# Kernel tuning notes

Measured on AMD Instinct MI355X. Metric: run time of the kernel, lower is better.

## Reference

```python
import jax, jax.numpy as jnp
import numpy as np

B, S, D_MODEL, N_HEADS, D_K, D_V = 2, 2048, 1024, 16, 64, 64


def setup_inputs() -> dict:
    key = jax.random.key(0)
    k1, k2, k3, k4, k5, k6, k7 = jax.random.split(key, 7)
    scale = 1.0 / np.sqrt(D_MODEL)
    inputs = {
        "input_Q": jax.random.normal(k1, (B, S, D_MODEL), dtype=jnp.float32),
        "input_K": jax.random.normal(k2, (B, S, D_MODEL), dtype=jnp.float32),
        "input_V": jax.random.normal(k3, (B, S, D_MODEL), dtype=jnp.float32),
        # causal mask: True means position is masked out (matches masked_fill_)
        "attn_mask": jnp.broadcast_to(
            ~jnp.tril(jnp.ones((S, S), dtype=bool)), (B, S, S)
        ),
        "flag": 0,
        "W_Q": jax.random.normal(k4, (D_MODEL, N_HEADS * D_K), dtype=jnp.float32) * scale,
        "W_K": jax.random.normal(k5, (D_MODEL, N_HEADS * D_K), dtype=jnp.float32) * scale,
        "W_V": jax.random.normal(k6, (D_MODEL, N_HEADS * D_V), dtype=jnp.float32) * scale,
        "W_O": jax.random.normal(k7, (N_HEADS * D_V, D_MODEL), dtype=jnp.float32) * scale,
    }
    return inputs


def reference(input_Q, input_K, input_V, attn_mask, flag, W_Q, W_K, W_V, W_O):
    b = input_Q.shape[0]
    # project and split heads: [b, h, s, d]
    Q = (input_Q @ W_Q).reshape(b, -1, N_HEADS, D_K).transpose(0, 2, 1, 3)
    K = (input_K @ W_K).reshape(b, -1, N_HEADS, D_K).transpose(0, 2, 1, 3)
    V = (input_V @ W_V).reshape(b, -1, N_HEADS, D_V).transpose(0, 2, 1, 3)
    # scaled dot-product attention with additive large-negative masking
    scores = jnp.einsum("bhqd,bhkd->bhqk", Q, K) / np.sqrt(D_K).astype(np.float32)
    scores = jnp.where(attn_mask[:, None, :, :], jnp.float32(-1e9), scores)
    attn = jax.nn.softmax(scores, axis=-1)
    context = jnp.einsum("bhqk,bhkd->bhqd", attn, V)  # [b, h, s, d_v]
    context = context.transpose(0, 2, 1, 3).reshape(b, -1, N_HEADS * D_V)
    return context @ W_O
```

## Files before the change

### kernel.cpp

```cpp
#include <hip/hip_runtime.h>

#define DEVINL __device__ __forceinline__

typedef __attribute__((ext_vector_type(8))) short short8;
typedef __attribute__((ext_vector_type(4))) float floatx4;

constexpr int S_LEN = 2048;
constexpr int DM    = 1024;
constexpr int NHEAD = 16;
constexpr int DHEAD = 64;
constexpr int BATCH = 2;
constexpr int MROWS = BATCH * S_LEN;
constexpr float LOG2E = 1.44269504f;
constexpr float SM_C1 = 0.125f * LOG2E;
constexpr float SM_C2 = -24.0f * LOG2E;

DEVINL unsigned short f2bf(float x) {
  union { float f; unsigned u; } un; un.f = x;
  unsigned u = un.u;
  return (unsigned short)((u + 0x7fffu + ((u >> 16) & 1u)) >> 16);
}
DEVINL unsigned short f2bf_fast(float x) {
  union { float f; unsigned u; } un; un.f = x;
  return (unsigned short)((un.u + 0x8000u) >> 16);
}

__global__ __launch_bounds__(256) void conv3_kernel(const float* __restrict__ s0,
                                                    const float* __restrict__ s1,
                                                    const float* __restrict__ s2,
                                                    unsigned short* __restrict__ d0,
                                                    unsigned short* __restrict__ d1,
                                                    unsigned short* __restrict__ d2) {
  const float* s = blockIdx.y == 0 ? s0 : (blockIdx.y == 1 ? s1 : s2);
  unsigned short* d = blockIdx.y == 0 ? d0 : (blockIdx.y == 1 ? d1 : d2);
  int i = (blockIdx.x * 256 + threadIdx.x) * 4;
  float4 v = *(const float4*)(s + i);
  unsigned lo = (unsigned)f2bf(v.x) | ((unsigned)f2bf(v.y) << 16);
  unsigned hi = (unsigned)f2bf(v.z) | ((unsigned)f2bf(v.w) << 16);
  *(uint2*)(d + i) = make_uint2(lo, hi);
}

__global__ __launch_bounds__(256) void trans4_kernel(const float* __restrict__ W0,
                                                     const float* __restrict__ W1,
                                                     const float* __restrict__ W2,
                                                     const float* __restrict__ W3,
                                                     unsigned short* __restrict__ T0,
                                                     unsigned short* __restrict__ T1,
                                                     unsigned short* __restrict__ T2,
                                                     unsigned short* __restrict__ T3) {
  const float* W = blockIdx.z == 0 ? W0 : (blockIdx.z == 1 ? W1 : (blockIdx.z == 2 ? W2 : W3));
  unsigned short* Wt = blockIdx.z == 0 ? T0 : (blockIdx.z == 1 ? T1 : (blockIdx.z == 2 ? T2 : T3));
  __shared__ unsigned short tile[32][33];
  int t = threadIdx.x;
  int c = t & 31, r0 = t >> 5;
  int nB = blockIdx.x * 32, kB = blockIdx.y * 32;
  for (int i = 0; i < 4; ++i) {
    int r = r0 + i * 8;
    tile[r][c] = f2bf(W[(size_t)(kB + r) * DM + nB + c]);
  }
  __syncthreads();
  for (int i = 0; i < 4; ++i) {
    int r = r0 + i * 8;
    Wt[(size_t)(nB + r) * DM + kB + c] = tile[c][r];
  }
}

__global__ __launch_bounds__(256) void vtrans_kernel(const unsigned short* __restrict__ vp,
                                                     unsigned short* __restrict__ vt) {
  const int bh = blockIdx.x;
  const int st = blockIdx.y;
  const int b = bh >> 4, h = bh & 15;
  const int s0 = st * 64;
  const int tid = threadIdx.x;
  __shared__ alignas(16) unsigned short tile[64 * 72];
#pragma unroll
  for (int j = 0; j < 2; ++j) {
    int ch = j * 256 + tid;
    int r = ch >> 3, c8 = (ch & 7) * 8;
    *(uint4*)&tile[r * 72 + c8] =
        *(const uint4*)&vp[((size_t)(b * S_LEN + s0 + r)) * DM + h * DHEAD + c8];
  }
  __syncthreads();
#pragma unroll
  for (int j = 0; j < 2; ++j) {
    int ch = j * 256 + tid;
    int d = ch >> 3, s8 = (ch & 7) * 8;
    unsigned short w[8];
#pragma unroll
    for (int e = 0; e < 8; ++e) w[e] = tile[(s8 + e) * 72 + d];
    *(uint4*)&vt[((size_t)(bh * DHEAD + d)) * S_LEN + s0 + s8] = *(const uint4*)w;
  }
}

DEVINL void load_lds16(const unsigned short* g, unsigned short* l) {
  __builtin_amdgcn_global_load_lds((const __attribute__((address_space(1))) unsigned int*)g,
                                   (__attribute__((address_space(3))) unsigned int*)l,
                                   16, 0, 0);
}

template <int MODE>
DEVINL void gemm_body(const unsigned short* __restrict__ A,
                      const unsigned short* __restrict__ Bt,
                      void* __restrict__ Cout) {
  constexpr int K = 1024, N = 1024;
  __shared__ alignas(16) unsigned short As[128 * 32];
  __shared__ alignas(16) unsigned short Bs[128 * 32];
  const int tid  = threadIdx.x;
  const int wave = tid >> 6, lane = tid & 63;
  const int quad = lane >> 4, l16 = lane & 15;
  const int mBase = blockIdx.y * 128, nBase = blockIdx.x * 128;
  const int wm = (wave >> 1) * 64, wn = (wave & 1) * 64;
  const int sr = lane >> 2;
  const int sc = (lane & 3) * 8;
  floatx4 acc[4][4] = {};

  for (int k0 = 0; k0 < K; k0 += 32) {
    __syncthreads();
#pragma unroll
    for (int j = 0; j < 2; ++j) {
      int row = wave * 32 + j * 16 + sr;
      load_lds16(A  + (size_t)(mBase + row) * K + k0 + sc, As + (wave * 32 + j * 16) * 32);
      load_lds16(Bt + (size_t)(nBase + row) * K + k0 + sc, Bs + (wave * 32 + j * 16) * 32);
    }
    __syncthreads();
    short8 af[4], bfr[4];
#pragma unroll
    for (int mt = 0; mt < 4; ++mt) af[mt]  = *(const short8*)&As[(wm + mt * 16 + l16) * 32 + quad * 8];
#pragma unroll
    for (int nt = 0; nt < 4; ++nt) bfr[nt] = *(const short8*)&Bs[(wn + nt * 16 + l16) * 32 + quad * 8];
#pragma unroll
    for (int mt = 0; mt < 4; ++mt)
#pragma unroll
      for (int nt = 0; nt < 4; ++nt)
        acc[mt][nt] = __builtin_amdgcn_mfma_f32_16x16x32_bf16(af[mt], bfr[nt], acc[mt][nt], 0, 0, 0);
  }

#pragma unroll
  for (int mt = 0; mt < 4; ++mt)
#pragma unroll
    for (int nt = 0; nt < 4; ++nt)
#pragma unroll
      for (int r = 0; r < 4; ++r) {
        int m = mBase + wm + mt * 16 + quad * 4 + r;
        int n = nBase + wn + nt * 16 + l16;
        if (MODE == 0) ((unsigned short*)Cout)[(size_t)m * N + n] = f2bf(acc[mt][nt][r]);
        else           ((float*)Cout)[(size_t)m * N + n]          = acc[mt][nt][r];
      }
}

__global__ __launch_bounds__(256) void gemm_qkv(const unsigned short* __restrict__ A0,
                                                const unsigned short* __restrict__ A1,
                                                const unsigned short* __restrict__ A2,
                                                const unsigned short* __restrict__ B0,
                                                const unsigned short* __restrict__ B1,
                                                const unsigned short* __restrict__ B2,
                                                unsigned short* __restrict__ C0,
                                                unsigned short* __restrict__ C1,
                                                unsigned short* __restrict__ C2) {
  const int z = blockIdx.z;
  const unsigned short* A  = z == 0 ? A0 : (z == 1 ? A1 : A2);
  const unsigned short* Bt = z == 0 ? B0 : (z == 1 ? B1 : B2);
  unsigned short* C        = z == 0 ? C0 : (z == 1 ? C1 : C2);
  gemm_body<0>(A, Bt, C);
}

__global__ __launch_bounds__(256) void gemm_out(const unsigned short* __restrict__ A,
                                                const unsigned short* __restrict__ Bt,
                                                float* __restrict__ C) {
  gemm_body<1>(A, Bt, C);
}

__global__ __launch_bounds__(256) void attn_kernel(const unsigned short* __restrict__ Qp,
                                                   const unsigned short* __restrict__ Kp,
                                                   const unsigned short* __restrict__ Vtg,
                                                   unsigned short* __restrict__ ctx) {
  const int qt = gridDim.x - 1 - blockIdx.x;
  const int bh = blockIdx.y;
  const int b  = bh >> 4, h = bh & 15;
  const int tid = threadIdx.x;
  const int wave = tid >> 6, lane = tid & 63;
  const int quad = lane >> 4, l16 = lane & 15;
  const int Q0 = qt * 128;
  const int nT = 2 * qt + 2;

  __shared__ alignas(16) unsigned short Ks[64 * 72];
  __shared__ alignas(16) unsigned short Vs[64 * 72];
  __shared__ alignas(16) unsigned short Ps[4][32 * 72];

  const unsigned short* Kbh = Kp  + (size_t)(b * S_LEN) * DM + h * DHEAD;
  const unsigned short* Vbh = Vtg + (size_t)(bh * DHEAD) * S_LEN;

  const int sr = tid >> 3, sc8 = (tid & 7) * 8;
  const unsigned short* kptr = Kbh + (size_t)sr * DM + sc8;
  const unsigned short* vptr = Vbh + (size_t)sr * S_LEN + sc8;
  unsigned short* ksl = Ks + sr * 72 + sc8;
  unsigned short* vsl = Vs + sr * 72 + sc8;

  const int rowbase = Q0 + wave * 32;
  short8 qf[2][2];
#pragma unroll
  for (int mt = 0; mt < 2; ++mt) {
    const size_t qrow = ((size_t)(b * S_LEN + rowbase + mt * 16 + l16)) * DM + h * DHEAD;
    qf[mt][0] = *(const short8*)&Qp[qrow + quad * 8];
    qf[mt][1] = *(const short8*)&Qp[qrow + 32 + quad * 8];
  }

  floatx4 o[2][4] = {};
  float rs[2][4] = {};
  unsigned short* Pw = &Ps[wave][0];

  uint4 kr0 = *(const uint4*)kptr;
  uint4 kr1 = *(const uint4*)(kptr + (size_t)32 * DM);
  uint4 vr0 = *(const uint4*)vptr;
  uint4 vr1 = *(const uint4*)(vptr + (size_t)32 * S_LEN);

  for (int t = 0; t < nT; ++t) {
    const int kb = t * 64;
    __syncthreads();
    *(uint4*)ksl              = kr0;
    *(uint4*)(ksl + 32 * 72)  = kr1;
    *(uint4*)vsl              = vr0;
    *(uint4*)(vsl + 32 * 72)  = vr1;
    __syncthreads();

    {
      const int kbn = (t + 1 < nT) ? (t + 1) * 64 : 0;
      kr0 = *(const uint4*)(kptr + (size_t)kbn * DM);
      kr1 = *(const uint4*)(kptr + (size_t)(kbn + 32) * DM);
      vr0 = *(const uint4*)(vptr + kbn);
      vr1 = *(const uint4*)(vptr + (size_t)32 * S_LEN + kbn);
    }

    floatx4 sc[2][4];
#pragma unroll
    for (int nt = 0; nt < 4; ++nt) {
      short8 kf0 = *(const short8*)&Ks[(nt * 16 + l16) * 72 + quad * 8];
      short8 kf1 = *(const short8*)&Ks[(nt * 16 + l16) * 72 + 32 + quad * 8];
#pragma unroll
      for (int mt = 0; mt < 2; ++mt) {
        floatx4 a = {};
        a = __builtin_amdgcn_mfma_f32_16x16x32_bf16(qf[mt][0], kf0, a, 0, 0, 0);
        a = __builtin_amdgcn_mfma_f32_16x16x32_bf16(qf[mt][1], kf1, a, 0, 0, 0);
        sc[mt][nt] = a;
      }
    }

    const bool masked = (t >= nT - 2);
#pragma unroll
    for (int mt = 0; mt < 2; ++mt)
#pragma unroll
      for (int nt = 0; nt < 4; ++nt) {
        const int colg = kb + nt * 16 + l16;
#pragma unroll
        for (int r = 0; r < 4; ++r) {
          float p = __builtin_amdgcn_exp2f(fmaf(sc[mt][nt][r], SM_C1, SM_C2));
          if (masked && colg > rowbase + mt * 16 + quad * 4 + r) p = 0.f;
          rs[mt][r] += p;
          Pw[(mt * 16 + quad * 4 + r) * 72 + nt * 16 + l16] = f2bf_fast(p);
        }
      }

    short8 vf[4][2];
#pragma unroll
    for (int dt = 0; dt < 4; ++dt) {
      vf[dt][0] = *(const short8*)&Vs[(dt * 16 + l16) * 72 + quad * 8];
      vf[dt][1] = *(const short8*)&Vs[(dt * 16 + l16) * 72 + 32 + quad * 8];
    }
#pragma unroll
    for (int mt = 0; mt < 2; ++mt) {
      short8 pf0 = *(const short8*)&Pw[(mt * 16 + l16) * 72 + quad * 8];
      short8 pf1 = *(const short8*)&Pw[(mt * 16 + l16) * 72 + 32 + quad * 8];
#pragma unroll
      for (int dt = 0; dt < 4; ++dt) {
        o[mt][dt] = __builtin_amdgcn_mfma_f32_16x16x32_bf16(pf0, vf[dt][0], o[mt][dt], 0, 0, 0);
        o[mt][dt] = __builtin_amdgcn_mfma_f32_16x16x32_bf16(pf1, vf[dt][1], o[mt][dt], 0, 0, 0);
      }
    }
  }

#pragma unroll
  for (int mt = 0; mt < 2; ++mt)
#pragma unroll
    for (int r = 0; r < 4; ++r) {
      float l = rs[mt][r];
#pragma unroll
      for (int off = 1; off < 16; off <<= 1) l += __shfl_xor(l, off, 64);
      float inv = 1.0f / l;
      const size_t row = (size_t)(b * S_LEN + rowbase + mt * 16 + quad * 4 + r);
#pragma unroll
      for (int dt = 0; dt < 4; ++dt)
        ctx[row * DM + h * DHEAD + dt * 16 + l16] = f2bf(o[mt][dt][r] * inv);
    }
}

extern "C" void kernel_launch(void* const* d_in, const int* in_sizes, int n_in,
                              void* d_out, int out_size, void* d_ws, size_t ws_size,
                              hipStream_t stream) {
  const float* Xq = (const float*)d_in[0];
  const float* Xk = (const float*)d_in[1];
  const float* Xv = (const float*)d_in[2];
  const float* Wq = (const float*)d_in[5];
  const float* Wk = (const float*)d_in[6];
  const float* Wv = (const float*)d_in[7];
  const float* Wo = (const float*)d_in[8];
  float* out = (float*)d_out;

  char* ws = (char*)d_ws;
  constexpr size_t XBYTES = (size_t)MROWS * DM * 2;
  constexpr size_t WBYTES = (size_t)DM * DM * 2;
  unsigned short* xq_bf = (unsigned short*)(ws);
  unsigned short* xk_bf = (unsigned short*)(ws + XBYTES);
  unsigned short* xv_bf = (unsigned short*)(ws + 2 * XBYTES);
  unsigned short* wqt   = (unsigned short*)(ws + 3 * XBYTES);
  unsigned short* wkt   = (unsigned short*)(ws + 3 * XBYTES + WBYTES);
  unsigned short* wvt   = (unsigned short*)(ws + 3 * XBYTES + 2 * WBYTES);
  unsigned short* wot   = (unsigned short*)(ws + 3 * XBYTES + 3 * WBYTES);
  unsigned short* qp    = (unsigned short*)(ws + 3 * XBYTES + 4 * WBYTES);
  unsigned short* kp    = (unsigned short*)(ws + 4 * XBYTES + 4 * WBYTES);
  unsigned short* vp    = (unsigned short*)(ws + 5 * XBYTES + 4 * WBYTES);
  unsigned short* ctx   = xq_bf;
  unsigned short* vt    = xk_bf;

  const int nX = MROWS * DM;
  conv3_kernel<<<dim3(nX / 1024, 3), 256, 0, stream>>>(Xq, Xk, Xv, xq_bf, xk_bf, xv_bf);
  trans4_kernel<<<dim3(32, 32, 4), 256, 0, stream>>>(Wq, Wk, Wv, Wo, wqt, wkt, wvt, wot);

  gemm_qkv<<<dim3(DM / 128, MROWS / 128, 3), 256, 0, stream>>>(
      xq_bf, xk_bf, xv_bf, wqt, wkt, wvt, qp, kp, vp);

  vtrans_kernel<<<dim3(BATCH * NHEAD, S_LEN / 64), 256, 0, stream>>>(vp, vt);

  attn_kernel<<<dim3(S_LEN / 128, BATCH * NHEAD), 256, 0, stream>>>(qp, kp, vt, ctx);

  gemm_out<<<dim3(DM / 128, MROWS / 128), 256, 0, stream>>>(ctx, wot, out);
}
```

Baseline: 270.5 us.

## Fuse V transpose into QKV GEMM, restructure attention to split keys across waves

```diff
diff --git a/kernel.cpp b/kernel.cpp
--- a/kernel.cpp
+++ b/kernel.cpp
@@ -3,6 +3,7 @@
 #define DEVINL __device__ __forceinline__
 
 typedef __attribute__((ext_vector_type(8))) short short8;
+typedef __attribute__((ext_vector_type(4))) short sh4;
 typedef __attribute__((ext_vector_type(4))) float floatx4;
 
 constexpr int S_LEN = 2048;
@@ -14,6 +15,8 @@
 constexpr float LOG2E = 1.44269504f;
 constexpr float SM_C1 = 0.125f * LOG2E;
 constexpr float SM_C2 = -24.0f * LOG2E;
+
+#define MFMA16(a, b, c) __builtin_amdgcn_mfma_f32_16x16x16bf16_1k(a, b, c, 0, 0, 0)
 
 DEVINL unsigned short f2bf(float x) {
   union { float f; unsigned u; } un; un.f = x;
@@ -65,33 +68,6 @@
   }
 }
 
-__global__ __launch_bounds__(256) void vtrans_kernel(const unsigned short* __restrict__ vp,
-                                                     unsigned short* __restrict__ vt) {
-  const int bh = blockIdx.x;
-  const int st = blockIdx.y;
-  const int b = bh >> 4, h = bh & 15;
-  const int s0 = st * 64;
-  const int tid = threadIdx.x;
-  __shared__ alignas(16) unsigned short tile[64 * 72];
-#pragma unroll
-  for (int j = 0; j < 2; ++j) {
-    int ch = j * 256 + tid;
-    int r = ch >> 3, c8 = (ch & 7) * 8;
-    *(uint4*)&tile[r * 72 + c8] =
-        *(const uint4*)&vp[((size_t)(b * S_LEN + s0 + r)) * DM + h * DHEAD + c8];
-  }
-  __syncthreads();
-#pragma unroll
-  for (int j = 0; j < 2; ++j) {
-    int ch = j * 256 + tid;
-    int d = ch >> 3, s8 = (ch & 7) * 8;
-    unsigned short w[8];
-#pragma unroll
-    for (int e = 0; e < 8; ++e) w[e] = tile[(s8 + e) * 72 + d];
-    *(uint4*)&vt[((size_t)(bh * DHEAD + d)) * S_LEN + s0 + s8] = *(const uint4*)w;
-  }
-}
-
 DEVINL void load_lds16(const unsigned short* g, unsigned short* l) {
   __builtin_amdgcn_global_load_lds((const __attribute__((address_space(1))) unsigned int*)g,
                                    (__attribute__((address_space(3))) unsigned int*)l,
@@ -138,14 +114,25 @@
 #pragma unroll
   for (int mt = 0; mt < 4; ++mt)
 #pragma unroll
-    for (int nt = 0; nt < 4; ++nt)
-#pragma unroll
-      for (int r = 0; r < 4; ++r) {
-        int m = mBase + wm + mt * 16 + quad * 4 + r;
-        int n = nBase + wn + nt * 16 + l16;
-        if (MODE == 0) ((unsigned short*)Cout)[(size_t)m * N + n] = f2bf(acc[mt][nt][r]);
-        else           ((float*)Cout)[(size_t)m * N + n]          = acc[mt][nt][r];
+    for (int nt = 0; nt < 4; ++nt) {
+      const int m = mBase + wm + mt * 16 + quad * 4;
+      const int n = nBase + wn + nt * 16 + l16;
+      if (MODE == 2) {
+        const int bq = m >> 11, s = m & 2047;
+        const int hh = n >> 6,  d = n & 63;
+        unsigned short w4[4];
+#pragma unroll
+        for (int r = 0; r < 4; ++r) w4[r] = f2bf(acc[mt][nt][r]);
+        *(uint2*)&((unsigned short*)Cout)[((size_t)((bq * 16 + hh) * 64 + d)) * S_LEN + s] =
+            *(const uint2*)w4;
+      } else {
+#pragma unroll
+        for (int r = 0; r < 4; ++r) {
+          if (MODE == 0) ((unsigned short*)Cout)[(size_t)(m + r) * N + n] = f2bf(acc[mt][nt][r]);
+          else           ((float*)Cout)[(size_t)(m + r) * N + n]          = acc[mt][nt][r];
+        }
       }
+    }
 }
 
 __global__ __launch_bounds__(256) void gemm_qkv(const unsigned short* __restrict__ A0,
@@ -158,139 +145,182 @@
                                                 unsigned short* __restrict__ C1,
                                                 unsigned short* __restrict__ C2) {
   const int z = blockIdx.z;
-  const unsigned short* A  = z == 0 ? A0 : (z == 1 ? A1 : A2);
-  const unsigned short* Bt = z == 0 ? B0 : (z == 1 ? B1 : B2);
-  unsigned short* C        = z == 0 ? C0 : (z == 1 ? C1 : C2);
-  gemm_body<0>(A, Bt, C);
-}
-
-__global__ __launch_bounds__(256) void gemm_out(const unsigned short* __restrict__ A,
-                                                const unsigned short* __restrict__ Bt,
-                                                float* __restrict__ C) {
-  gemm_body<1>(A, Bt, C);
-}
-
-__global__ __launch_bounds__(256) void attn_kernel(const unsigned short* __restrict__ Qp,
-                                                   const unsigned short* __restrict__ Kp,
-                                                   const unsigned short* __restrict__ Vtg,
-                                                   unsigned short* __restrict__ ctx) {
-  const int qt = gridDim.x - 1 - blockIdx.x;
+  if (z == 2)      gemm_body<2>(A2, B2, C2);
+  else if (z == 1) gemm_body<0>(A1, B1, C1);
+  else             gemm_body<0>(A0, B0, C0);
+}
+
+__global__ __launch_bounds__(256) void gemm_out64(const unsigned short* __restrict__ A,
+                                                  const unsigned short* __restrict__ Bt,
+                                                  float* __restrict__ C) {
+  constexpr int K = 1024, N = 1024;
+  __shared__ alignas(16) unsigned short As[64 * 32];
+  __shared__ alignas(16) unsigned short Bs[128 * 32];
+  const int tid  = threadIdx.x;
+  const int wave = tid >> 6, lane = tid & 63;
+  const int quad = lane >> 4, l16 = lane & 15;
+  const int mBase = blockIdx.y * 64, nBase = blockIdx.x * 128;
+  const int wm = (wave >> 1) * 32, wn = (wave & 1) * 64;
+  const int sr = lane >> 2;
+  const int sc = (lane & 3) * 8;
+  floatx4 acc[2][4] = {};
+
+  for (int k0 = 0; k0 < K; k0 += 32) {
+    __syncthreads();
+    load_lds16(A + (size_t)(mBase + wave * 16 + sr) * K + k0 + sc, As + (wave * 16) * 32);
+#pragma unroll
+    for (int j = 0; j < 2; ++j) {
+      int row = wave * 32 + j * 16 + sr;
+      load_lds16(Bt + (size_t)(nBase + row) * K + k0 + sc, Bs + (wave * 32 + j * 16) * 32);
+    }
+    __syncthreads();
+    short8 af[2], bfr[4];
+#pragma unroll
+    for (int mt = 0; mt < 2; ++mt) af[mt]  = *(const short8*)&As[(wm + mt * 16 + l16) * 32 + quad * 8];
+#pragma unroll
+    for (int nt = 0; nt < 4; ++nt) bfr[nt] = *(const short8*)&Bs[(wn + nt * 16 + l16) * 32 + quad * 8];
+#pragma unroll
+    for (int mt = 0; mt < 2; ++mt)
+#pragma unroll
+      for (int nt = 0; nt < 4; ++nt)
+        acc[mt][nt] = __builtin_amdgcn_mfma_f32_16x16x32_bf16(af[mt], bfr[nt], acc[mt][nt], 0, 0, 0);
+  }
+
+#pragma unroll
+  for (int mt = 0; mt < 2; ++mt)
+#pragma unroll
+    for (int nt = 0; nt < 4; ++nt)
+#pragma unroll
+      for (int r = 0; r < 4; ++r) {
+        int m = mBase + wm + mt * 16 + quad * 4 + r;
+        int n = nBase + wn + nt * 16 + l16;
+        C[(size_t)m * N + n] = acc[mt][nt][r];
+      }
+}
+
+__global__ __launch_bounds__(256, 3) void attn_kernel(const unsigned short* __restrict__ Qp,
+                                                      const unsigned short* __restrict__ Kp,
+                                                      const unsigned short* __restrict__ Vtg,
+                                                      unsigned short* __restrict__ ctx) {
+  const int qt = 31 - blockIdx.x;
   const int bh = blockIdx.y;
   const int b  = bh >> 4, h = bh & 15;
   const int tid = threadIdx.x;
-  const int wave = tid >> 6, lane = tid & 63;
+  const int w = tid >> 6, lane = tid & 63;
   const int quad = lane >> 4, l16 = lane & 15;
-  const int Q0 = qt * 128;
-  const int nT = 2 * qt + 2;
-
-  __shared__ alignas(16) unsigned short Ks[64 * 72];
-  __shared__ alignas(16) unsigned short Vs[64 * 72];
-  __shared__ alignas(16) unsigned short Ps[4][32 * 72];
-
-  const unsigned short* Kbh = Kp  + (size_t)(b * S_LEN) * DM + h * DHEAD;
-  const unsigned short* Vbh = Vtg + (size_t)(bh * DHEAD) * S_LEN;
-
-  const int sr = tid >> 3, sc8 = (tid & 7) * 8;
-  const unsigned short* kptr = Kbh + (size_t)sr * DM + sc8;
-  const unsigned short* vptr = Vbh + (size_t)sr * S_LEN + sc8;
-  unsigned short* ksl = Ks + sr * 72 + sc8;
-  unsigned short* vsl = Vs + sr * 72 + sc8;
-
-  const int rowbase = Q0 + wave * 32;
-  short8 qf[2][2];
-#pragma unroll
-  for (int mt = 0; mt < 2; ++mt) {
-    const size_t qrow = ((size_t)(b * S_LEN + rowbase + mt * 16 + l16)) * DM + h * DHEAD;
-    qf[mt][0] = *(const short8*)&Qp[qrow + quad * 8];
-    qf[mt][1] = *(const short8*)&Qp[qrow + 32 + quad * 8];
-  }
-
-  floatx4 o[2][4] = {};
-  float rs[2][4] = {};
-  unsigned short* Pw = &Ps[wave][0];
-
-  uint4 kr0 = *(const uint4*)kptr;
-  uint4 kr1 = *(const uint4*)(kptr + (size_t)32 * DM);
-  uint4 vr0 = *(const uint4*)vptr;
-  uint4 vr1 = *(const uint4*)(vptr + (size_t)32 * S_LEN);
-
-  for (int t = 0; t < nT; ++t) {
+  const int Q0 = qt * 64;
+  const int nT = qt + 1;
+
+  short8 qB[4][2];
+#pragma unroll
+  for (int nt = 0; nt < 4; ++nt) {
+    const size_t qr = ((size_t)(b * S_LEN + Q0 + nt * 16 + l16)) * DM + h * DHEAD + quad * 8;
+    qB[nt][0] = *(const short8*)&Qp[qr];
+    qB[nt][1] = *(const short8*)&Qp[qr + 32];
+  }
+
+  const unsigned short* kptr = Kp + ((size_t)(b * S_LEN) + w * 16 + l16) * DM + h * DHEAD + quad * 8;
+  const unsigned short* vptr = Vtg + ((size_t)(bh * DHEAD) + l16) * S_LEN + w * 16 + quad * 4;
+
+  floatx4 o[4][4] = {};
+  float rs[4] = {0.f, 0.f, 0.f, 0.f};
+
+  short8 kc0 = *(const short8*)kptr;
+  short8 kc1 = *(const short8*)(kptr + 32);
+
+  for (int t = 0; t < nT - 1; ++t) {
     const int kb = t * 64;
-    __syncthreads();
-    *(uint4*)ksl              = kr0;
-    *(uint4*)(ksl + 32 * 72)  = kr1;
-    *(uint4*)vsl              = vr0;
-    *(uint4*)(vsl + 32 * 72)  = vr1;
-    __syncthreads();
-
-    {
-      const int kbn = (t + 1 < nT) ? (t + 1) * 64 : 0;
-      kr0 = *(const uint4*)(kptr + (size_t)kbn * DM);
-      kr1 = *(const uint4*)(kptr + (size_t)(kbn + 32) * DM);
-      vr0 = *(const uint4*)(vptr + kbn);
-      vr1 = *(const uint4*)(vptr + (size_t)32 * S_LEN + kbn);
-    }
-
-    floatx4 sc[2][4];
+    sh4 vv[4];
+#pragma unroll
+    for (int dt = 0; dt < 4; ++dt)
+      vv[dt] = *(const sh4*)(vptr + (size_t)(dt * 16) * S_LEN + kb);
+    short8 kn0 = *(const short8*)(kptr + (size_t)(kb + 64) * DM);
+    short8 kn1 = *(const short8*)(kptr + (size_t)(kb + 64) * DM + 32);
+
 #pragma unroll
     for (int nt = 0; nt < 4; ++nt) {
-      short8 kf0 = *(const short8*)&Ks[(nt * 16 + l16) * 72 + quad * 8];
-      short8 kf1 = *(const short8*)&Ks[(nt * 16 + l16) * 72 + 32 + quad * 8];
-#pragma unroll
-      for (int mt = 0; mt < 2; ++mt) {
-        floatx4 a = {};
-        a = __builtin_amdgcn_mfma_f32_16x16x32_bf16(qf[mt][0], kf0, a, 0, 0, 0);
-        a = __builtin_amdgcn_mfma_f32_16x16x32_bf16(qf[mt][1], kf1, a, 0, 0, 0);
-        sc[mt][nt] = a;
+      floatx4 sc = {};
+      sc = __builtin_amdgcn_mfma_f32_16x16x32_bf16(kc0, qB[nt][0], sc, 0, 0, 0);
+      sc = __builtin_amdgcn_mfma_f32_16x16x32_bf16(kc1, qB[nt][1], sc, 0, 0, 0);
+      sh4 pa;
+      float acc = 0.f;
+#pragma unroll
+      for (int r = 0; r < 4; ++r) {
+        float p = __builtin_amdgcn_exp2f(fmaf(sc[r], SM_C1, SM_C2));
+        acc += p;
+        pa[r] = (short)f2bf_fast(p);
       }
-    }
-
-    const bool masked = (t >= nT - 2);
-#pragma unroll
-    for (int mt = 0; mt < 2; ++mt)
-#pragma unroll
-      for (int nt = 0; nt < 4; ++nt) {
-        const int colg = kb + nt * 16 + l16;
-#pragma unroll
-        for (int r = 0; r < 4; ++r) {
-          float p = __builtin_amdgcn_exp2f(fmaf(sc[mt][nt][r], SM_C1, SM_C2));
-          if (masked && colg > rowbase + mt * 16 + quad * 4 + r) p = 0.f;
-          rs[mt][r] += p;
-          Pw[(mt * 16 + quad * 4 + r) * 72 + nt * 16 + l16] = f2bf_fast(p);
-        }
+      rs[nt] += acc;
+#pragma unroll
+      for (int dt = 0; dt < 4; ++dt)
+        o[nt][dt] = MFMA16(pa, vv[dt], o[nt][dt]);
+    }
+    kc0 = kn0; kc1 = kn1;
+  }
+
+  {
+    const int kb = Q0;
+    sh4 vv[4];
+#pragma unroll
+    for (int dt = 0; dt < 4; ++dt)
+      vv[dt] = *(const sh4*)(vptr + (size_t)(dt * 16) * S_LEN + kb);
+    const int sbase = w * 16 + quad * 4;
+#pragma unroll
+    for (int nt = 0; nt < 4; ++nt) {
+      floatx4 sc = {};
+      sc = __builtin_amdgcn_mfma_f32_16x16x32_bf16(kc0, qB[nt][0], sc, 0, 0, 0);
+      sc = __builtin_amdgcn_mfma_f32_16x16x32_bf16(kc1, qB[nt][1], sc, 0, 0, 0);
+      const int qoff = nt * 16 + l16;
+      sh4 pa;
+      float acc = 0.f;
+#pragma unroll
+      for (int r = 0; r < 4; ++r) {
+        float p = __builtin_amdgcn_exp2f(fmaf(sc[r], SM_C1, SM_C2));
+        if (sbase + r > qoff) p = 0.f;
+        acc += p;
+        pa[r] = (short)f2bf_fast(p);
       }
-
-    short8 vf[4][2];
-#pragma unroll
-    for (int dt = 0; dt < 4; ++dt) {
-      vf[dt][0] = *(const short8*)&Vs[(dt * 16 + l16) * 72 + quad * 8];
-      vf[dt][1] = *(const short8*)&Vs[(dt * 16 + l16) * 72 + 32 + quad * 8];
-    }
-#pragma unroll
-    for (int mt = 0; mt < 2; ++mt) {
-      short8 pf0 = *(const short8*)&Pw[(mt * 16 + l16) * 72 + quad * 8];
-      short8 pf1 = *(const short8*)&Pw[(mt * 16 + l16) * 72 + 32 + quad * 8];
-#pragma unroll
-      for (int dt = 0; dt < 4; ++dt) {
-        o[mt][dt] = __builtin_amdgcn_mfma_f32_16x16x32_bf16(pf0, vf[dt][0], o[mt][dt], 0, 0, 0);
-        o[mt][dt] = __builtin_amdgcn_mfma_f32_16x16x32_bf16(pf1, vf[dt][1], o[mt][dt], 0, 0, 0);
-      }
-    }
-  }
-
-#pragma unroll
-  for (int mt = 0; mt < 2; ++mt)
-#pragma unroll
-    for (int r = 0; r < 4; ++r) {
-      float l = rs[mt][r];
-#pragma unroll
-      for (int off = 1; off < 16; off <<= 1) l += __shfl_xor(l, off, 64);
-      float inv = 1.0f / l;
-      const size_t row = (size_t)(b * S_LEN + rowbase + mt * 16 + quad * 4 + r);
+      rs[nt] += acc;
 #pragma unroll
       for (int dt = 0; dt < 4; ++dt)
-        ctx[row * DM + h * DHEAD + dt * 16 + l16] = f2bf(o[mt][dt][r] * inv);
-    }
+        o[nt][dt] = MFMA16(pa, vv[dt], o[nt][dt]);
+    }
+  }
+
+  __shared__ float rsL[4][4][16];
+  __shared__ alignas(16) float Ored[4][4][16][16];
+
+#pragma unroll
+  for (int nt = 0; nt < 4; ++nt) {
+    rs[nt] += __shfl_xor(rs[nt], 16, 64);
+    rs[nt] += __shfl_xor(rs[nt], 32, 64);
+  }
+  if (quad == 0) {
+#pragma unroll
+    for (int nt = 0; nt < 4; ++nt) rsL[w][nt][l16] = rs[nt];
+  }
+
+  for (int nt = 0; nt < 4; ++nt) {
+    __syncthreads();
+#pragma unroll
+    for (int dt = 0; dt < 4; ++dt)
+      *(floatx4*)&Ored[w][dt][l16][quad * 4] = o[nt][dt];
+    __syncthreads();
+    floatx4 acc = {};
+#pragma unroll
+    for (int w2 = 0; w2 < 4; ++w2) {
+      floatx4 v = *(const floatx4*)&Ored[w2][w][l16][quad * 4];
+#pragma unroll
+      for (int j = 0; j < 4; ++j) acc[j] += v[j];
+    }
+#pragma unroll
+    for (int j = 0; j < 4; ++j) {
+      const int q16 = quad * 4 + j;
+      float l = rsL[0][nt][q16] + rsL[1][nt][q16] + rsL[2][nt][q16] + rsL[3][nt][q16];
+      const size_t row = (size_t)(b * S_LEN + Q0 + nt * 16 + q16);
+      ctx[row * DM + h * DHEAD + w * 16 + l16] = f2bf(acc[j] / l);
+    }
+  }
 }
 
 extern "C" void kernel_launch(void* const* d_in, const int* in_sizes, int n_in,
@@ -317,20 +347,17 @@
   unsigned short* wot   = (unsigned short*)(ws + 3 * XBYTES + 3 * WBYTES);
   unsigned short* qp    = (unsigned short*)(ws + 3 * XBYTES + 4 * WBYTES);
   unsigned short* kp    = (unsigned short*)(ws + 4 * XBYTES + 4 * WBYTES);
-  unsigned short* vp    = (unsigned short*)(ws + 5 * XBYTES + 4 * WBYTES);
+  unsigned short* vt    = (unsigned short*)(ws + 5 * XBYTES + 4 * WBYTES);
   unsigned short* ctx   = xq_bf;
-  unsigned short* vt    = xk_bf;
 
   const int nX = MROWS * DM;
   conv3_kernel<<<dim3(nX / 1024, 3), 256, 0, stream>>>(Xq, Xk, Xv, xq_bf, xk_bf, xv_bf);
   trans4_kernel<<<dim3(32, 32, 4), 256, 0, stream>>>(Wq, Wk, Wv, Wo, wqt, wkt, wvt, wot);
 
   gemm_qkv<<<dim3(DM / 128, MROWS / 128, 3), 256, 0, stream>>>(
-      xq_bf, xk_bf, xv_bf, wqt, wkt, wvt, qp, kp, vp);
-
-  vtrans_kernel<<<dim3(BATCH * NHEAD, S_LEN / 64), 256, 0, stream>>>(vp, vt);
-
-  attn_kernel<<<dim3(S_LEN / 128, BATCH * NHEAD), 256, 0, stream>>>(qp, kp, vt, ctx);
-
-  gemm_out<<<dim3(DM / 128, MROWS / 128), 256, 0, stream>>>(ctx, wot, out);
-}
+      xq_bf, xk_bf, xv_bf, wqt, wkt, wvt, qp, kp, vt);
+
+  attn_kernel<<<dim3(32, BATCH * NHEAD), 256, 0, stream>>>(qp, kp, vt, ctx);
+
+  gemm_out64<<<dim3(DM / 128, MROWS / 64), 256, 0, stream>>>(ctx, wot, out);
+}
```

Result: slower. 291.1 us (+7.6%).
